# Kernel tuning notes

Hardware: AMD Instinct MI355X
Metric: run time of the kernel (lower is better)

Reference implementation:

```python
import jax, jax.numpy as jnp
import numpy as np

BLK = 128            # weight_block_size for w8a16 blockwise dequant
H = 1024             # hidden_size
I = 512              # moe_intermediate_size
E = 64               # n_routed_experts
T = 512              # tokens (seq_len)
K = 6                # num_experts_per_tok
G = 8                # n_group
TG = 3               # topk_group
NSH = 2              # n_shared_experts
I2 = I * NSH         # shared expert intermediate size
ROUTED_SCALE = 2.5
NORM_TOPK = True


def dq(w_int8, scale, blk=BLK):
    """Blockwise w8a16 dequant: w [..., M, N] int8, scale [..., M/blk, N/blk] f32."""
    *lead, M, N = w_int8.shape
    w = w_int8.astype(scale.dtype).reshape(*lead, M // blk, blk, N // blk, blk)
    return (w * scale[..., :, None, :, None]).reshape(*lead, M, N)


def setup_inputs() -> dict:
    key = jax.random.key(0)
    ks = jax.random.split(key, 16)
    ri = lambda k, shp: jax.random.randint(k, shp, -8, 8, dtype=jnp.int8)
    rs = lambda k, shp: jax.random.uniform(k, shp, minval=0.01, maxval=0.03, dtype=jnp.float32)
    return {
        "x": jax.random.normal(ks[0], (T, H), jnp.float32),
        "gate_w": jax.random.normal(ks[1], (E, H), jnp.float32) * 0.02,  # router gate [E,H]
        "wg": ri(ks[2], (E, I, H)),  "sg": rs(ks[3], (E, I // BLK, H // BLK)),
        "wu": ri(ks[4], (E, I, H)),  "su": rs(ks[5], (E, I // BLK, H // BLK)),
        "wd": ri(ks[6], (E, I, H)),  "sd": rs(ks[7], (E, I // BLK, H // BLK)),  # down, transposed layout [I,H]
        "sh_wg": ri(ks[8], (I2, H)),  "sh_sg": rs(ks[9], (I2 // BLK, H // BLK)),
        "sh_wu": ri(ks[10], (I2, H)), "sh_su": rs(ks[11], (I2 // BLK, H // BLK)),
        "sh_wd": ri(ks[12], (I2, H)), "sh_sd": rs(ks[13], (I2 // BLK, H // BLK)),
    }


def _moe(x, gate_w, wg, sg, wu, su, wd, sd, sh_wg, sh_sg, sh_wu, sh_su, sh_wd, sh_sd):
    Tn = x.shape[0]
    # --- router: sigmoid scoring + group-limited top-k ---
    scores = jax.nn.sigmoid(x @ gate_w.T)                       # [T, E]
    gsz = E // G
    group_scores = scores.reshape(Tn, G, gsz).max(axis=-1)      # [T, G]
    _, gidx = jax.lax.top_k(group_scores, TG)                   # [T, TG]
    gmask = jax.nn.one_hot(gidx, G, dtype=scores.dtype).sum(1)  # [T, G]
    emask = jnp.repeat(gmask, gsz, axis=-1)                     # [T, E]
    masked = jnp.where(emask > 0, scores, -jnp.inf)
    w, idx = jax.lax.top_k(masked, K)                           # [T, K]
    if NORM_TOPK:
        w = w / (w.sum(-1, keepdims=True) + 1e-20)
    w = w * ROUTED_SCALE
    # per-token combine weights over experts
    comb = (jax.nn.one_hot(idx, E, dtype=x.dtype) * w[:, :, None]).sum(1)  # [T, E]

    # --- routed experts: dequantized silu-gated MLPs, masked dense combine ---
    Wg, Wu, Wd = dq(wg, sg), dq(wu, su), dq(wd, sd)             # [E, I, H]
    g = jnp.einsum('th,eih->eti', x, Wg)                        # [E, T, I]
    u = jnp.einsum('th,eih->eti', x, Wu)
    hmid = jax.nn.silu(g) * u
    y = jnp.einsum('eti,eih->eth', hmid, Wd)                    # [E, T, H]
    routed = jnp.einsum('eth,te->th', y, comb)                  # [T, H]

    # --- shared experts MLP ---
    Sg, Su, Sd = dq(sh_wg, sh_sg), dq(sh_wu, sh_su), dq(sh_wd, sh_sd)
    shared = (jax.nn.silu(x @ Sg.T) * (x @ Su.T)) @ Sd          # [T, H]
    return routed + shared


def reference(x, gate_w, wg, sg, wu, su, wd, sd, sh_wg, sh_sg, sh_wu, sh_su, sh_wd, sh_sd):
    return _moe(x, gate_w, wg, sg, wu, su, wd, sd,
                sh_wg, sh_sg, sh_wu, sh_su, sh_wd, sh_sd)
```

## Files before the change

### kernel.cpp

```cpp
#include <hip/hip_runtime.h>
#include <math.h>
#include <stdint.h>

#define T_   512
#define H_   1024
#define I_   512
#define E_   64
#define K_   6
#define G_   8
#define TG_  3
#define EB_  80

typedef _Float16 h8 __attribute__((ext_vector_type(8)));
typedef _Float16 h4v __attribute__((ext_vector_type(4)));
typedef float    f4 __attribute__((ext_vector_type(4)));

__global__ __launch_bounds__(64) void router_k(
    const float* __restrict__ x, const float* __restrict__ gw,
    int* __restrict__ cnt, int* __restrict__ tlist, float* __restrict__ wlist)
{
  const int t   = blockIdx.x;
  const int tid = threadIdx.x;
  __shared__ float sx[H_];
  __shared__ float sc[E_];

  for (int h4 = tid; h4 < H_/4; h4 += 64)
    ((float4*)sx)[h4] = ((const float4*)(x + (size_t)t*H_))[h4];
  __syncthreads();

  const float* wr = gw + (size_t)tid * H_;
  float acc = 0.f;
  for (int h = 0; h < H_; h += 4) {
    float4 xv = *(const float4*)(sx + h);
    float4 wv = *(const float4*)(wr + h);
    acc = fmaf(xv.x, wv.x, acc); acc = fmaf(xv.y, wv.y, acc);
    acc = fmaf(xv.z, wv.z, acc); acc = fmaf(xv.w, wv.w, acc);
  }
  sc[tid] = 1.f / (1.f + expf(-acc));
  __syncthreads();

  if (tid == 0) {
    float gs[G_];
    #pragma unroll
    for (int g = 0; g < G_; g++) {
      float m = sc[g*8];
      #pragma unroll
      for (int j = 1; j < 8; j++) m = fmaxf(m, sc[g*8+j]);
      gs[g] = m;
    }
    unsigned gp = 0;
    for (int r = 0; r < TG_; r++) {
      int best = 0; float bv = -1e30f;
      for (int g = 0; g < G_; g++)
        if (!((gp >> g) & 1) && gs[g] > bv) { bv = gs[g]; best = g; }
      gp |= 1u << best;
    }
    int   eidx[K_]; float ew[K_];
    unsigned long long em = 0ull;
    float wsum = 0.f;
    for (int r = 0; r < K_; r++) {
      int best = 0; float bv = -1e30f;
      for (int e = 0; e < E_; e++) {
        if (!((gp >> (e >> 3)) & 1)) continue;
        if ((em >> e) & 1ull) continue;
        if (sc[e] > bv) { bv = sc[e]; best = e; }
      }
      em |= 1ull << best; eidx[r] = best; ew[r] = bv; wsum += bv;
    }
    const float inv = 2.5f / (wsum + 1e-20f);
    for (int r = 0; r < K_; r++) {
      int e = eidx[r];
      int pos = atomicAdd(&cnt[e], 1);
      tlist[e*T_ + pos] = (t << 13) | (t*K_ + r);
      wlist[e*T_ + pos] = ew[r] * inv;
    }
  }
}

__global__ void pseudo_init_k(int* cnt, int* tlist, float* wlist) {
  int s = blockIdx.x*256 + threadIdx.x;
  if (s == 0) { cnt[64] = T_; cnt[65] = T_; }
  if (s < 1024) {
    int e = 64 + (s >> 9);
    int t = s & 511;
    tlist[e*T_ + t] = (t << 13) | (3072 + s);
    wlist[e*T_ + t] = 1.0f;
  }
}

__global__ __launch_bounds__(256) void xh_prep_k(
    const float* __restrict__ x, _Float16* __restrict__ xh)
{
  int i = blockIdx.x*256 + threadIdx.x;
  float4 v = ((const float4*)x)[i];
  h4v o = { (_Float16)v.x, (_Float16)v.y, (_Float16)v.z, (_Float16)v.w };
  *(h4v*)(xh + (size_t)i*4) = o;
}

__device__ __forceinline__ void eb_decode(int eb, const int* cnt,
                                          int& e, int& lo, int& hi) {
  if (eb < E_) { e = eb; lo = 0; hi = cnt[e]; }
  else { int q = (eb - E_) & 7; e = E_ + ((eb - E_) >> 3); lo = q*64; hi = lo + 64; }
}

__device__ __forceinline__ h8 cvt8(int4 a, int4 b, float s) {
  union { _Float16 f[8]; h8 v; } t;
  t.f[0]=(_Float16)((float)a.x*s); t.f[1]=(_Float16)((float)a.y*s);
  t.f[2]=(_Float16)((float)a.z*s); t.f[3]=(_Float16)((float)a.w*s);
  t.f[4]=(_Float16)((float)b.x*s); t.f[5]=(_Float16)((float)b.y*s);
  t.f[6]=(_Float16)((float)b.z*s); t.f[7]=(_Float16)((float)b.w*s);
  return t.v;
}

#define NKT_G 32

#define GU_STEP(KT, WN)                                                       \
  do {                                                                        \
    asm volatile("s_waitcnt vmcnt(" #WN ") lgkmcnt(0)" ::: "memory");         \
    __builtin_amdgcn_sched_barrier(0);                                        \
    __builtin_amdgcn_s_barrier();                                             \
    __builtin_amdgcn_sched_barrier(0);                                        \
    if ((KT) + 1 < NKT_G)                                                     \
      *(h8*)(wdst + (((KT)+1)&1)*5120) =                                      \
          cvt8(Wr[((KT)+1)%3][0], Wr[((KT)+1)%3][1], sv[((KT)+1)>>2]);        \
    if ((KT) + 3 < NKT_G) {                                                   \
      Wr[((KT)+3)%3][0] = *(const int4*)(wsrc + ((KT)+3)*32);                 \
      Wr[((KT)+3)%3][1] = *(const int4*)(wsrc + ((KT)+3)*32 + 4);             \
    }                                                                         \
    {                                                                         \
      const _Float16* tb = lds0 + ((KT)&1)*5120;                              \
      h8 bg0 = *(const h8*)(tb + ro0);                                        \
      h8 bg1 = *(const h8*)(tb + ro1);                                        \
      h8 bu0 = *(const h8*)(tb + 2560 + ro0);                                 \
      h8 bu1 = *(const h8*)(tb + 2560 + ro1);                                 \
      accg0 = __builtin_amdgcn_mfma_f32_16x16x32_f16(Ar[(KT)%4], bg0, accg0, 0,0,0); \
      accg1 = __builtin_amdgcn_mfma_f32_16x16x32_f16(Ar[(KT)%4], bg1, accg1, 0,0,0); \
      accu0 = __builtin_amdgcn_mfma_f32_16x16x32_f16(Ar[(KT)%4], bu0, accu0, 0,0,0); \
      accu1 = __builtin_amdgcn_mfma_f32_16x16x32_f16(Ar[(KT)%4], bu1, accu1, 0,0,0); \
    }                                                                         \
    if ((KT) + 3 < NKT_G)                                                     \
      Ar[((KT)+3)%4] = *(const h8*)(ax + ((KT)+3)*32);                        \
  } while (0)

__global__ __launch_bounds__(512, 6) void gateup_k(
    const _Float16* __restrict__ xh,
    const int* __restrict__ wg, const float* __restrict__ sg,
    const int* __restrict__ wu, const float* __restrict__ su,
    const int* __restrict__ shwg, const float* __restrict__ shsg,
    const int* __restrict__ shwu, const float* __restrict__ shsu,
    const int* __restrict__ cnt, const int* __restrict__ tlist,
    const float* __restrict__ wlist,
    _Float16* __restrict__ hmid)
{
  const int ic = blockIdx.x;
  const int eb = blockIdx.y;
  int e, lo, hi;
  eb_decode(eb, cnt, e, lo, hi);
  if (hi <= lo) return;

  const int tid  = threadIdx.x;
  const int lane = tid & 63;
  const int wv   = tid >> 6;
  const int mr   = lane & 15;
  const int quad = lane >> 4;
  const int wm   = wv & 3;
  const int wn   = wv >> 2;

  const int *wgb, *wub; const float *sgp, *sup; int sib;
  if (e < E_) {
    wgb = wg + (size_t)e*I_*H_;  wub = wu + (size_t)e*I_*H_;
    sgp = sg + e*32;  sup = su + e*32;  sib = ic >> 1;
  } else {
    int hf = e - E_;
    wgb = shwg + (size_t)hf*512*H_;  wub = shwu + (size_t)hf*512*H_;
    sgp = shsg;  sup = shsu;  sib = hf*4 + (ic >> 1);
  }

  const int smat = tid >> 8;
  const int sr   = (tid >> 2) & 63;
  const int sseg = tid & 3;
  const int* wsrc = (smat ? wub : wgb) + (size_t)(ic*64 + sr)*H_ + sseg*8;
  const float* ssc = (smat ? sup : sgp) + sib*8;
  float sv[8];
  #pragma unroll
  for (int b = 0; b < 8; b++) sv[b] = ssc[b];

  __shared__ _Float16 wlds[2*2*64*40];
  __shared__ int stok[64]; __shared__ int srw[64]; __shared__ float swt[64];
  _Float16* lds0 = wlds;
  _Float16* wdst = wlds + smat*2560 + sr*40 + sseg*8;
  const int ro0 = (wn*32 + mr)*40 + quad*8;
  const int ro1 = ro0 + 16*40;

  int4 Wr[3][2];
  h8   Ar[4];

  for (int base = lo; base < hi; base += 64) {
    __syncthreads();
    if (tid < 64) {
      int slot = base + tid;
      if (slot < hi) {
        int ent = tlist[e*T_ + slot];
        stok[tid] = ent >> 13; srw[tid] = ent & 8191; swt[tid] = wlist[e*T_ + slot];
      } else { stok[tid] = -1; srw[tid] = 0; swt[tid] = 0.f; }
    }
    __syncthreads();

    int tk = stok[wm*16 + mr]; if (tk < 0) tk = 0;
    const _Float16* ax = xh + (size_t)tk*H_ + quad*8;

    f4 accg0 = (f4){0.f,0.f,0.f,0.f}, accg1 = accg0, accu0 = accg0, accu1 = accg0;

    Wr[0][0] = *(const int4*)(wsrc);      Wr[0][1] = *(const int4*)(wsrc + 4);
    Ar[0]    = *(const h8*)(ax);
    Wr[1][0] = *(const int4*)(wsrc + 32); Wr[1][1] = *(const int4*)(wsrc + 36);
    Ar[1]    = *(const h8*)(ax + 32);
    Wr[2][0] = *(const int4*)(wsrc + 64); Wr[2][1] = *(const int4*)(wsrc + 68);
    Ar[2]    = *(const h8*)(ax + 64);
    asm volatile("s_waitcnt vmcnt(7)" ::: "memory");
    __builtin_amdgcn_sched_barrier(0);
    *(h8*)(wdst) = cvt8(Wr[0][0], Wr[0][1], sv[0]);

    GU_STEP(0,4);  GU_STEP(1,4);  GU_STEP(2,4);  GU_STEP(3,4);
    GU_STEP(4,4);  GU_STEP(5,4);  GU_STEP(6,4);  GU_STEP(7,4);
    GU_STEP(8,4);  GU_STEP(9,4);  GU_STEP(10,4); GU_STEP(11,4);
    GU_STEP(12,4); GU_STEP(13,4); GU_STEP(14,4); GU_STEP(15,4);
    GU_STEP(16,4); GU_STEP(17,4); GU_STEP(18,4); GU_STEP(19,4);
    GU_STEP(20,4); GU_STEP(21,4); GU_STEP(22,4); GU_STEP(23,4);
    GU_STEP(24,4); GU_STEP(25,4); GU_STEP(26,4); GU_STEP(27,4);
    GU_STEP(28,4); GU_STEP(29,4); GU_STEP(30,1); GU_STEP(31,0);

    const int icol = ic*64 + wn*32 + mr;
    #pragma unroll
    for (int r = 0; r < 4; r++) {
      int sl = wm*16 + quad*4 + r;
      if (stok[sl] >= 0) {
        float wt = swt[sl];
        float g0 = accg0[r];
        float m0 = g0 / (1.f + expf(-g0)) * accu0[r] * wt;
        float g1 = accg1[r];
        float m1 = g1 / (1.f + expf(-g1)) * accu1[r] * wt;
        _Float16* hp = hmid + (size_t)srw[sl]*I_ + icol;
        hp[0]  = (_Float16)m0;
        hp[16] = (_Float16)m1;
      }
    }
  }
}
#undef GU_STEP

#define NKT_D 16

#define DN_LDW(S, KT)                                                         \
  do {                                                                        \
    Wr[S][0] = *(const int2*)(dsrc + (size_t)((KT)*32 + 0)*H_);               \
    Wr[S][1] = *(const int2*)(dsrc + (size_t)((KT)*32 + 1)*H_);               \
    Wr[S][2] = *(const int2*)(dsrc + (size_t)((KT)*32 + 2)*H_);               \
    Wr[S][3] = *(const int2*)(dsrc + (size_t)((KT)*32 + 3)*H_);               \
  } while (0)

#define DN_WRITE(S, BUF, SC)                                                  \
  do {                                                                        \
    union { _Float16 f[4]; h4v v; } v0, v1;                                   \
    v0.f[0]=(_Float16)((float)Wr[S][0].x*(SC)); v0.f[1]=(_Float16)((float)Wr[S][1].x*(SC)); \
    v0.f[2]=(_Float16)((float)Wr[S][2].x*(SC)); v0.f[3]=(_Float16)((float)Wr[S][3].x*(SC)); \
    v1.f[0]=(_Float16)((float)Wr[S][0].y*(SC)); v1.f[1]=(_Float16)((float)Wr[S][1].y*(SC)); \
    v1.f[2]=(_Float16)((float)Wr[S][2].y*(SC)); v1.f[3]=(_Float16)((float)Wr[S][3].y*(SC)); \
    *(h4v*)(ddst0 + (BUF)*2560)      = v0.v;                                  \
    *(h4v*)(ddst0 + (BUF)*2560 + 40) = v1.v;                                  \
  } while (0)

#define DN_STEP(KT, WN)                                                       \
  do {                                                                        \
    asm volatile("s_waitcnt vmcnt(" #WN ") lgkmcnt(0)" ::: "memory");         \
    __builtin_amdgcn_sched_barrier(0);                                        \
    __builtin_amdgcn_s_barrier();                                             \
    __builtin_amdgcn_sched_barrier(0);                                        \
    if ((KT) + 1 < NKT_D) DN_WRITE(((KT)+1)%3, ((KT)+1)&1, scd[((KT)+1)>>2]); \
    if ((KT) + 3 < NKT_D) DN_LDW(((KT)+3)%3, (KT)+3);                         \
    {                                                                         \
      const _Float16* tb = lds0 + ((KT)&1)*2560;                              \
      h8 b0 = *(const h8*)(tb + ro0);                                         \
      h8 b1 = *(const h8*)(tb + ro1);                                         \
      h8 b2 = *(const h8*)(tb + ro2);                                         \
      h8 b3 = *(const h8*)(tb + ro3);                                         \
      tot0 = __builtin_amdgcn_mfma_f32_16x16x32_f16(Ar[(KT)%4], b0, tot0, 0,0,0); \
      tot1 = __builtin_amdgcn_mfma_f32_16x16x32_f16(Ar[(KT)%4], b1, tot1, 0,0,0); \
      tot2 = __builtin_amdgcn_mfma_f32_16x16x32_f16(Ar[(KT)%4], b2, tot2, 0,0,0); \
      tot3 = __builtin_amdgcn_mfma_f32_16x16x32_f16(Ar[(KT)%4], b3, tot3, 0,0,0); \
    }                                                                         \
    if ((KT) + 3 < NKT_D)                                                     \
      Ar[((KT)+3)%4] = *(const h8*)(ap + ((KT)+3)*32);                        \
  } while (0)

__global__ __launch_bounds__(256, 6) void down_k(
    const int* __restrict__ wd, const float* __restrict__ sd,
    const int* __restrict__ shwd, const float* __restrict__ shsd,
    const int* __restrict__ cnt, const int* __restrict__ tlist,
    const _Float16* __restrict__ hmid, float* __restrict__ scr)
{
  const int hc = blockIdx.x;
  const int eb = blockIdx.y;
  int e, lo, hi;
  eb_decode(eb, cnt, e, lo, hi);
  if (hi <= lo) return;

  const int tid  = threadIdx.x;
  const int lane = tid & 63;
  const int wv   = tid >> 6;
  const int mr   = lane & 15;
  const int quad = lane >> 4;

  const int* wb; const float* sdp; int sib0;
  if (e < E_) { wb = wd + (size_t)e*I_*H_;        sdp = sd + e*32;  sib0 = 0; }
  else { int hf = e - E_; wb = shwd + (size_t)hf*512*H_; sdp = shsd; sib0 = hf*4; }
  float scd[4];
  #pragma unroll
  for (int ib = 0; ib < 4; ib++) scd[ib] = sdp[(sib0+ib)*8 + (hc >> 1)];

  const int ig = tid >> 5;
  const int hp = tid & 31;
  const int* dsrc = wb + (size_t)(ig*4)*H_ + hc*64 + hp*2;

  __shared__ _Float16 wlds[2*64*40];
  __shared__ int stok[64]; __shared__ int srw[64];
  _Float16* lds0  = wlds;
  _Float16* ddst0 = wlds + (hp*2)*40 + ig*4;
  const int ro0 = (     mr)*40 + quad*8;
  const int ro1 = (16 + mr)*40 + quad*8;
  const int ro2 = (32 + mr)*40 + quad*8;
  const int ro3 = (48 + mr)*40 + quad*8;

  int2 Wr[3][4];
  h8   Ar[4];

  for (int base = lo; base < hi; base += 64) {
    __syncthreads();
    if (tid < 64) {
      int slot = base + tid;
      if (slot < hi) {
        int ent = tlist[e*T_ + slot];
        stok[tid] = ent >> 13; srw[tid] = ent & 8191;
      } else { stok[tid] = -1; srw[tid] = 0; }
    }
    __syncthreads();

    const _Float16* ap = hmid + (size_t)srw[wv*16 + mr]*I_ + quad*8;

    f4 tot0 = (f4){0.f,0.f,0.f,0.f}, tot1 = tot0, tot2 = tot0, tot3 = tot0;

    DN_LDW(0, 0); Ar[0] = *(const h8*)(ap);
    DN_LDW(1, 1); Ar[1] = *(const h8*)(ap + 32);
    DN_LDW(2, 2); Ar[2] = *(const h8*)(ap + 64);
    asm volatile("s_waitcnt vmcnt(10)" ::: "memory");
    __builtin_amdgcn_sched_barrier(0);
    DN_WRITE(0, 0, scd[0]);

    DN_STEP(0,6);  DN_STEP(1,6);  DN_STEP(2,6);  DN_STEP(3,6);
    DN_STEP(4,6);  DN_STEP(5,6);  DN_STEP(6,6);  DN_STEP(7,6);
    DN_STEP(8,6);  DN_STEP(9,6);  DN_STEP(10,6); DN_STEP(11,6);
    DN_STEP(12,6); DN_STEP(13,6); DN_STEP(14,1); DN_STEP(15,0);

    #pragma unroll
    for (int r = 0; r < 4; r++) {
      int sl = wv*16 + quad*4 + r;
      if (stok[sl] >= 0) {
        int t  = stok[sl];
        int sr = srw[sl];
        int rank = (sr < 3072) ? (sr - t*6) : (6 + ((sr - 3072) >> 9));
        float* dst = scr + (size_t)(t*8 + rank)*H_ + hc*64 + mr;
        dst[0]  = tot0[r];
        dst[16] = tot1[r];
        dst[32] = tot2[r];
        dst[48] = tot3[r];
      }
    }
  }
}
#undef DN_STEP
#undef DN_WRITE
#undef DN_LDW

__global__ __launch_bounds__(256) void combine_k(
    const float* __restrict__ scr, float* __restrict__ out)
{
  int i = blockIdx.x*256 + threadIdx.x;
  int t = i >> 8;
  int c = i & 255;
  const float4* base = (const float4*)(scr + (size_t)t*8*H_) + c;
  float4 s = base[0];
  #pragma unroll
  for (int r = 1; r < 8; r++) {
    float4 v = base[(size_t)r*(H_/4)];
    s.x += v.x; s.y += v.y; s.z += v.z; s.w += v.w;
  }
  ((float4*)out)[i] = s;
}

extern "C" void kernel_launch(void* const* d_in, const int* in_sizes, int n_in,
                              void* d_out, int out_size, void* d_ws, size_t ws_size,
                              hipStream_t stream) {
  (void)in_sizes; (void)n_in; (void)ws_size; (void)out_size;
  const float* x    = (const float*)d_in[0];
  const float* gw   = (const float*)d_in[1];
  const int*   wg   = (const int*  )d_in[2];
  const float* sg   = (const float*)d_in[3];
  const int*   wu   = (const int*  )d_in[4];
  const float* su   = (const float*)d_in[5];
  const int*   wd   = (const int*  )d_in[6];
  const float* sd   = (const float*)d_in[7];
  const int*   shwg = (const int*  )d_in[8];
  const float* shsg = (const float*)d_in[9];
  const int*   shwu = (const int*  )d_in[10];
  const float* shsu = (const float*)d_in[11];
  const int*   shwd = (const int*  )d_in[12];
  const float* shsd = (const float*)d_in[13];
  float* out = (float*)d_out;

  char* ws = (char*)d_ws;
  int*      cnt   = (int*     ) ws;
  int*      tlist = (int*     )(ws + 1024);
  float*    wlist = (float*   )(ws + 1024 + 66*T_*4);
  _Float16* hmid  = (_Float16*)(ws + 1024 + 2*66*T_*4);
  _Float16* xh    = (_Float16*)(ws + 1024 + 2*66*T_*4 + 4096*I_*2);
  float*    scr   = (float*   )(ws + 1024 + 2*66*T_*4 + 4096*I_*2 + T_*H_*2);

  hipMemsetAsync(cnt, 0, 1024, stream);
  xh_prep_k<<<T_*H_/1024, 256, 0, stream>>>(x, xh);
  router_k<<<T_, 64, 0, stream>>>(x, gw, cnt, tlist, wlist);
  pseudo_init_k<<<4, 256, 0, stream>>>(cnt, tlist, wlist);
  gateup_k<<<dim3(8, EB_), 512, 0, stream>>>(xh, wg, sg, wu, su,
                                             shwg, shsg, shwu, shsu,
                                             cnt, tlist, wlist, hmid);
  down_k<<<dim3(16, EB_), 256, 0, stream>>>(wd, sd, shwd, shsd,
                                            cnt, tlist, hmid, scr);
  combine_k<<<T_*H_/1024, 256, 0, stream>>>(scr, out);
}
```

Before: 557.3 us.

## Halve gate/up and down column tiles and fold prep kernels into router

Gate/up blocks now cover 32 intermediate columns instead of 64, and down blocks cover 32 hidden columns instead of 64. Each launch therefore has twice as many blocks with fewer accumulators and registers each, and the occupancy hint rises to 8. The fp16 conversion of x and the shared-expert pseudo-routing setup move into the router kernel, which removes two launches. Routing weights are now stored per (token, rank) row instead of per expert slot. In exchange, each block rereads the activation tiles for fewer output columns, which raises redundant A-operand traffic and the number of barriers per FLOP.

```diff
diff --git a/kernel.cpp b/kernel.cpp
--- a/kernel.cpp
+++ b/kernel.cpp
@@ -13,11 +13,13 @@
 
 typedef _Float16 h8 __attribute__((ext_vector_type(8)));
 typedef _Float16 h4v __attribute__((ext_vector_type(4)));
+typedef _Float16 h2v __attribute__((ext_vector_type(2)));
 typedef float    f4 __attribute__((ext_vector_type(4)));
 
 __global__ __launch_bounds__(64) void router_k(
     const float* __restrict__ x, const float* __restrict__ gw,
-    int* __restrict__ cnt, int* __restrict__ tlist, float* __restrict__ wlist)
+    int* __restrict__ cnt, int* __restrict__ tlist,
+    float* __restrict__ wrow, _Float16* __restrict__ xh)
 {
   const int t   = blockIdx.x;
   const int tid = threadIdx.x;
@@ -27,6 +29,20 @@
   for (int h4 = tid; h4 < H_/4; h4 += 64)
     ((float4*)sx)[h4] = ((const float4*)(x + (size_t)t*H_))[h4];
   __syncthreads();
+
+  for (int h4 = tid; h4 < H_/4; h4 += 64) {
+    float4 v = ((const float4*)sx)[h4];
+    h4v o = { (_Float16)v.x, (_Float16)v.y, (_Float16)v.z, (_Float16)v.w };
+    *(h4v*)(xh + (size_t)t*H_ + h4*4) = o;
+  }
+  if (t < 16) {
+    int s  = t*64 + tid;
+    int e  = 64 + (s >> 9);
+    int tt = s & 511;
+    tlist[e*T_ + tt] = (tt << 13) | (3072 + s);
+    wrow[3072 + s] = 1.0f;
+    if (s == 0) { cnt[64] = T_; cnt[65] = T_; }
+  }
 
   const float* wr = gw + (size_t)tid * H_;
   float acc = 0.f;
@@ -72,29 +88,9 @@
       int e = eidx[r];
       int pos = atomicAdd(&cnt[e], 1);
       tlist[e*T_ + pos] = (t << 13) | (t*K_ + r);
-      wlist[e*T_ + pos] = ew[r] * inv;
-    }
-  }
-}
-
-__global__ void pseudo_init_k(int* cnt, int* tlist, float* wlist) {
-  int s = blockIdx.x*256 + threadIdx.x;
-  if (s == 0) { cnt[64] = T_; cnt[65] = T_; }
-  if (s < 1024) {
-    int e = 64 + (s >> 9);
-    int t = s & 511;
-    tlist[e*T_ + t] = (t << 13) | (3072 + s);
-    wlist[e*T_ + t] = 1.0f;
-  }
-}
-
-__global__ __launch_bounds__(256) void xh_prep_k(
-    const float* __restrict__ x, _Float16* __restrict__ xh)
-{
-  int i = blockIdx.x*256 + threadIdx.x;
-  float4 v = ((const float4*)x)[i];
-  h4v o = { (_Float16)v.x, (_Float16)v.y, (_Float16)v.z, (_Float16)v.w };
-  *(h4v*)(xh + (size_t)i*4) = o;
+      wrow[t*K_ + r] = ew[r] * inv;
+    }
+  }
 }
 
 __device__ __forceinline__ void eb_decode(int eb, const int* cnt,
@@ -103,13 +99,10 @@
   else { int q = (eb - E_) & 7; e = E_ + ((eb - E_) >> 3); lo = q*64; hi = lo + 64; }
 }
 
-__device__ __forceinline__ h8 cvt8(int4 a, int4 b, float s) {
-  union { _Float16 f[8]; h8 v; } t;
-  t.f[0]=(_Float16)((float)a.x*s); t.f[1]=(_Float16)((float)a.y*s);
-  t.f[2]=(_Float16)((float)a.z*s); t.f[3]=(_Float16)((float)a.w*s);
-  t.f[4]=(_Float16)((float)b.x*s); t.f[5]=(_Float16)((float)b.y*s);
-  t.f[6]=(_Float16)((float)b.z*s); t.f[7]=(_Float16)((float)b.w*s);
-  return t.v;
+__device__ __forceinline__ h4v cvt4i(int4 w, float s) {
+  h4v t = { (_Float16)((float)w.x*s), (_Float16)((float)w.y*s),
+            (_Float16)((float)w.z*s), (_Float16)((float)w.w*s) };
+  return t;
 }
 
 #define NKT_G 32
@@ -121,38 +114,32 @@
     __builtin_amdgcn_s_barrier();                                             \
     __builtin_amdgcn_sched_barrier(0);                                        \
     if ((KT) + 1 < NKT_G)                                                     \
-      *(h8*)(wdst + (((KT)+1)&1)*5120) =                                      \
-          cvt8(Wr[((KT)+1)%3][0], Wr[((KT)+1)%3][1], sv[((KT)+1)>>2]);        \
-    if ((KT) + 3 < NKT_G) {                                                   \
-      Wr[((KT)+3)%3][0] = *(const int4*)(wsrc + ((KT)+3)*32);                 \
-      Wr[((KT)+3)%3][1] = *(const int4*)(wsrc + ((KT)+3)*32 + 4);             \
-    }                                                                         \
+      *(h4v*)(wdst + (((KT)+1)&1)*2560) =                                     \
+          cvt4i(Wr[((KT)+1)%3], sv[((KT)+1)>>2]);                             \
+    if ((KT) + 3 < NKT_G)                                                     \
+      Wr[((KT)+3)%3] = *(const int4*)(wsrc + ((KT)+3)*32);                    \
     {                                                                         \
-      const _Float16* tb = lds0 + ((KT)&1)*5120;                              \
-      h8 bg0 = *(const h8*)(tb + ro0);                                        \
-      h8 bg1 = *(const h8*)(tb + ro1);                                        \
-      h8 bu0 = *(const h8*)(tb + 2560 + ro0);                                 \
-      h8 bu1 = *(const h8*)(tb + 2560 + ro1);                                 \
-      accg0 = __builtin_amdgcn_mfma_f32_16x16x32_f16(Ar[(KT)%4], bg0, accg0, 0,0,0); \
-      accg1 = __builtin_amdgcn_mfma_f32_16x16x32_f16(Ar[(KT)%4], bg1, accg1, 0,0,0); \
-      accu0 = __builtin_amdgcn_mfma_f32_16x16x32_f16(Ar[(KT)%4], bu0, accu0, 0,0,0); \
-      accu1 = __builtin_amdgcn_mfma_f32_16x16x32_f16(Ar[(KT)%4], bu1, accu1, 0,0,0); \
+      const _Float16* tb = lds0 + ((KT)&1)*2560;                              \
+      h8 bg = *(const h8*)(tb + ro0);                                         \
+      h8 bu = *(const h8*)(tb + 1280 + ro0);                                  \
+      accg = __builtin_amdgcn_mfma_f32_16x16x32_f16(Ar[(KT)%4], bg, accg, 0,0,0); \
+      accu = __builtin_amdgcn_mfma_f32_16x16x32_f16(Ar[(KT)%4], bu, accu, 0,0,0); \
     }                                                                         \
     if ((KT) + 3 < NKT_G)                                                     \
       Ar[((KT)+3)%4] = *(const h8*)(ax + ((KT)+3)*32);                        \
   } while (0)
 
-__global__ __launch_bounds__(512, 6) void gateup_k(
+__global__ __launch_bounds__(512, 8) void gateup_k(
     const _Float16* __restrict__ xh,
     const int* __restrict__ wg, const float* __restrict__ sg,
     const int* __restrict__ wu, const float* __restrict__ su,
     const int* __restrict__ shwg, const float* __restrict__ shsg,
     const int* __restrict__ shwu, const float* __restrict__ shsu,
     const int* __restrict__ cnt, const int* __restrict__ tlist,
-    const float* __restrict__ wlist,
+    const float* __restrict__ wrow,
     _Float16* __restrict__ hmid)
 {
-  const int ic = blockIdx.x;
+  const int bi = blockIdx.x;
   const int eb = blockIdx.y;
   int e, lo, hi;
   eb_decode(eb, cnt, e, lo, hi);
@@ -169,30 +156,29 @@
   const int *wgb, *wub; const float *sgp, *sup; int sib;
   if (e < E_) {
     wgb = wg + (size_t)e*I_*H_;  wub = wu + (size_t)e*I_*H_;
-    sgp = sg + e*32;  sup = su + e*32;  sib = ic >> 1;
+    sgp = sg + e*32;  sup = su + e*32;  sib = bi >> 2;
   } else {
     int hf = e - E_;
     wgb = shwg + (size_t)hf*512*H_;  wub = shwu + (size_t)hf*512*H_;
-    sgp = shsg;  sup = shsu;  sib = hf*4 + (ic >> 1);
+    sgp = shsg;  sup = shsu;  sib = hf*4 + (bi >> 2);
   }
 
   const int smat = tid >> 8;
-  const int sr   = (tid >> 2) & 63;
-  const int sseg = tid & 3;
-  const int* wsrc = (smat ? wub : wgb) + (size_t)(ic*64 + sr)*H_ + sseg*8;
+  const int sr   = (tid >> 3) & 31;
+  const int seg  = tid & 7;
+  const int* wsrc = (smat ? wub : wgb) + (size_t)(bi*32 + sr)*H_ + seg*4;
   const float* ssc = (smat ? sup : sgp) + sib*8;
   float sv[8];
   #pragma unroll
   for (int b = 0; b < 8; b++) sv[b] = ssc[b];
 
-  __shared__ _Float16 wlds[2*2*64*40];
+  __shared__ _Float16 wlds[2*2*32*40];
   __shared__ int stok[64]; __shared__ int srw[64]; __shared__ float swt[64];
   _Float16* lds0 = wlds;
-  _Float16* wdst = wlds + smat*2560 + sr*40 + sseg*8;
-  const int ro0 = (wn*32 + mr)*40 + quad*8;
-  const int ro1 = ro0 + 16*40;
-
-  int4 Wr[3][2];
+  _Float16* wdst = wlds + smat*1280 + sr*40 + seg*4;
+  const int ro0 = (wn*16 + mr)*40 + quad*8;
+
+  int4 Wr[3];
   h8   Ar[4];
 
   for (int base = lo; base < hi; base += 64) {
@@ -201,7 +187,8 @@
       int slot = base + tid;
       if (slot < hi) {
         int ent = tlist[e*T_ + slot];
-        stok[tid] = ent >> 13; srw[tid] = ent & 8191; swt[tid] = wlist[e*T_ + slot];
+        stok[tid] = ent >> 13; srw[tid] = ent & 8191;
+        swt[tid]  = wrow[ent & 8191];
       } else { stok[tid] = -1; srw[tid] = 0; swt[tid] = 0.f; }
     }
     __syncthreads();
@@ -209,40 +196,33 @@
     int tk = stok[wm*16 + mr]; if (tk < 0) tk = 0;
     const _Float16* ax = xh + (size_t)tk*H_ + quad*8;
 
-    f4 accg0 = (f4){0.f,0.f,0.f,0.f}, accg1 = accg0, accu0 = accg0, accu1 = accg0;
-
-    Wr[0][0] = *(const int4*)(wsrc);      Wr[0][1] = *(const int4*)(wsrc + 4);
-    Ar[0]    = *(const h8*)(ax);
-    Wr[1][0] = *(const int4*)(wsrc + 32); Wr[1][1] = *(const int4*)(wsrc + 36);
-    Ar[1]    = *(const h8*)(ax + 32);
-    Wr[2][0] = *(const int4*)(wsrc + 64); Wr[2][1] = *(const int4*)(wsrc + 68);
-    Ar[2]    = *(const h8*)(ax + 64);
-    asm volatile("s_waitcnt vmcnt(7)" ::: "memory");
+    f4 accg = (f4){0.f,0.f,0.f,0.f}, accu = accg;
+
+    Wr[0] = *(const int4*)(wsrc);        Ar[0] = *(const h8*)(ax);
+    Wr[1] = *(const int4*)(wsrc + 32);   Ar[1] = *(const h8*)(ax + 32);
+    Wr[2] = *(const int4*)(wsrc + 64);   Ar[2] = *(const h8*)(ax + 64);
+    asm volatile("s_waitcnt vmcnt(5)" ::: "memory");
     __builtin_amdgcn_sched_barrier(0);
-    *(h8*)(wdst) = cvt8(Wr[0][0], Wr[0][1], sv[0]);
-
-    GU_STEP(0,4);  GU_STEP(1,4);  GU_STEP(2,4);  GU_STEP(3,4);
-    GU_STEP(4,4);  GU_STEP(5,4);  GU_STEP(6,4);  GU_STEP(7,4);
-    GU_STEP(8,4);  GU_STEP(9,4);  GU_STEP(10,4); GU_STEP(11,4);
-    GU_STEP(12,4); GU_STEP(13,4); GU_STEP(14,4); GU_STEP(15,4);
-    GU_STEP(16,4); GU_STEP(17,4); GU_STEP(18,4); GU_STEP(19,4);
-    GU_STEP(20,4); GU_STEP(21,4); GU_STEP(22,4); GU_STEP(23,4);
-    GU_STEP(24,4); GU_STEP(25,4); GU_STEP(26,4); GU_STEP(27,4);
-    GU_STEP(28,4); GU_STEP(29,4); GU_STEP(30,1); GU_STEP(31,0);
-
-    const int icol = ic*64 + wn*32 + mr;
+    *(h4v*)(wdst) = cvt4i(Wr[0], sv[0]);
+
+    GU_STEP(0,3);  GU_STEP(1,3);  GU_STEP(2,3);  GU_STEP(3,3);
+    GU_STEP(4,3);  GU_STEP(5,3);  GU_STEP(6,3);  GU_STEP(7,3);
+    GU_STEP(8,3);  GU_STEP(9,3);  GU_STEP(10,3); GU_STEP(11,3);
+    GU_STEP(12,3); GU_STEP(13,3); GU_STEP(14,3); GU_STEP(15,3);
+    GU_STEP(16,3); GU_STEP(17,3); GU_STEP(18,3); GU_STEP(19,3);
+    GU_STEP(20,3); GU_STEP(21,3); GU_STEP(22,3); GU_STEP(23,3);
+    GU_STEP(24,3); GU_STEP(25,3); GU_STEP(26,3); GU_STEP(27,3);
+    GU_STEP(28,3); GU_STEP(29,3); GU_STEP(30,1); GU_STEP(31,0);
+
+    const int icol = bi*32 + wn*16 + mr;
     #pragma unroll
     for (int r = 0; r < 4; r++) {
       int sl = wm*16 + quad*4 + r;
       if (stok[sl] >= 0) {
         float wt = swt[sl];
-        float g0 = accg0[r];
-        float m0 = g0 / (1.f + expf(-g0)) * accu0[r] * wt;
-        float g1 = accg1[r];
-        float m1 = g1 / (1.f + expf(-g1)) * accu1[r] * wt;
-        _Float16* hp = hmid + (size_t)srw[sl]*I_ + icol;
-        hp[0]  = (_Float16)m0;
-        hp[16] = (_Float16)m1;
+        float g0 = accg[r];
+        float m0 = g0 / (1.f + expf(-g0)) * accu[r] * wt;
+        hmid[(size_t)srw[sl]*I_ + icol] = (_Float16)m0;
       }
     }
   }
@@ -255,19 +235,16 @@
   do {                                                                        \
     Wr[S][0] = *(const int2*)(dsrc + (size_t)((KT)*32 + 0)*H_);               \
     Wr[S][1] = *(const int2*)(dsrc + (size_t)((KT)*32 + 1)*H_);               \
-    Wr[S][2] = *(const int2*)(dsrc + (size_t)((KT)*32 + 2)*H_);               \
-    Wr[S][3] = *(const int2*)(dsrc + (size_t)((KT)*32 + 3)*H_);               \
   } while (0)
 
 #define DN_WRITE(S, BUF, SC)                                                  \
   do {                                                                        \
-    union { _Float16 f[4]; h4v v; } v0, v1;                                   \
-    v0.f[0]=(_Float16)((float)Wr[S][0].x*(SC)); v0.f[1]=(_Float16)((float)Wr[S][1].x*(SC)); \
-    v0.f[2]=(_Float16)((float)Wr[S][2].x*(SC)); v0.f[3]=(_Float16)((float)Wr[S][3].x*(SC)); \
-    v1.f[0]=(_Float16)((float)Wr[S][0].y*(SC)); v1.f[1]=(_Float16)((float)Wr[S][1].y*(SC)); \
-    v1.f[2]=(_Float16)((float)Wr[S][2].y*(SC)); v1.f[3]=(_Float16)((float)Wr[S][3].y*(SC)); \
-    *(h4v*)(ddst0 + (BUF)*2560)      = v0.v;                                  \
-    *(h4v*)(ddst0 + (BUF)*2560 + 40) = v1.v;                                  \
+    h2v v0 = { (_Float16)((float)Wr[S][0].x*(SC)),                            \
+               (_Float16)((float)Wr[S][1].x*(SC)) };                          \
+    h2v v1 = { (_Float16)((float)Wr[S][0].y*(SC)),                            \
+               (_Float16)((float)Wr[S][1].y*(SC)) };                          \
+    *(h2v*)(ddst0 + (BUF)*1280)      = v0;                                    \
+    *(h2v*)(ddst0 + (BUF)*1280 + 40) = v1;                                    \
   } while (0)
 
 #define DN_STEP(KT, WN)                                                       \
@@ -279,21 +256,17 @@
     if ((KT) + 1 < NKT_D) DN_WRITE(((KT)+1)%3, ((KT)+1)&1, scd[((KT)+1)>>2]); \
     if ((KT) + 3 < NKT_D) DN_LDW(((KT)+3)%3, (KT)+3);                         \
     {                                                                         \
-      const _Float16* tb = lds0 + ((KT)&1)*2560;                              \
+      const _Float16* tb = lds0 + ((KT)&1)*1280;                              \
       h8 b0 = *(const h8*)(tb + ro0);                                         \
       h8 b1 = *(const h8*)(tb + ro1);                                         \
-      h8 b2 = *(const h8*)(tb + ro2);                                         \
-      h8 b3 = *(const h8*)(tb + ro3);                                         \
       tot0 = __builtin_amdgcn_mfma_f32_16x16x32_f16(Ar[(KT)%4], b0, tot0, 0,0,0); \
       tot1 = __builtin_amdgcn_mfma_f32_16x16x32_f16(Ar[(KT)%4], b1, tot1, 0,0,0); \
-      tot2 = __builtin_amdgcn_mfma_f32_16x16x32_f16(Ar[(KT)%4], b2, tot2, 0,0,0); \
-      tot3 = __builtin_amdgcn_mfma_f32_16x16x32_f16(Ar[(KT)%4], b3, tot3, 0,0,0); \
     }                                                                         \
     if ((KT) + 3 < NKT_D)                                                     \
       Ar[((KT)+3)%4] = *(const h8*)(ap + ((KT)+3)*32);                        \
   } while (0)
 
-__global__ __launch_bounds__(256, 6) void down_k(
+__global__ __launch_bounds__(256, 8) void down_k(
     const int* __restrict__ wd, const float* __restrict__ sd,
     const int* __restrict__ shwd, const float* __restrict__ shsd,
     const int* __restrict__ cnt, const int* __restrict__ tlist,
@@ -316,22 +289,20 @@
   else { int hf = e - E_; wb = shwd + (size_t)hf*512*H_; sdp = shsd; sib0 = hf*4; }
   float scd[4];
   #pragma unroll
-  for (int ib = 0; ib < 4; ib++) scd[ib] = sdp[(sib0+ib)*8 + (hc >> 1)];
-
-  const int ig = tid >> 5;
-  const int hp = tid & 31;
-  const int* dsrc = wb + (size_t)(ig*4)*H_ + hc*64 + hp*2;
-
-  __shared__ _Float16 wlds[2*64*40];
+  for (int ib = 0; ib < 4; ib++) scd[ib] = sdp[(sib0+ib)*8 + (hc >> 2)];
+
+  const int ig = tid >> 4;
+  const int hp = tid & 15;
+  const int* dsrc = wb + (size_t)(ig*2)*H_ + hc*32 + hp*2;
+
+  __shared__ _Float16 wlds[2*32*40];
   __shared__ int stok[64]; __shared__ int srw[64];
   _Float16* lds0  = wlds;
-  _Float16* ddst0 = wlds + (hp*2)*40 + ig*4;
+  _Float16* ddst0 = wlds + (hp*2)*40 + ig*2;
   const int ro0 = (     mr)*40 + quad*8;
   const int ro1 = (16 + mr)*40 + quad*8;
-  const int ro2 = (32 + mr)*40 + quad*8;
-  const int ro3 = (48 + mr)*40 + quad*8;
-
-  int2 Wr[3][4];
+
+  int2 Wr[3][2];
   h8   Ar[4];
 
   for (int base = lo; base < hi; base += 64) {
@@ -347,19 +318,19 @@
 
     const _Float16* ap = hmid + (size_t)srw[wv*16 + mr]*I_ + quad*8;
 
-    f4 tot0 = (f4){0.f,0.f,0.f,0.f}, tot1 = tot0, tot2 = tot0, tot3 = tot0;
+    f4 tot0 = (f4){0.f,0.f,0.f,0.f}, tot1 = tot0;
 
     DN_LDW(0, 0); Ar[0] = *(const h8*)(ap);
     DN_LDW(1, 1); Ar[1] = *(const h8*)(ap + 32);
     DN_LDW(2, 2); Ar[2] = *(const h8*)(ap + 64);
-    asm volatile("s_waitcnt vmcnt(10)" ::: "memory");
+    asm volatile("s_waitcnt vmcnt(7)" ::: "memory");
     __builtin_amdgcn_sched_barrier(0);
     DN_WRITE(0, 0, scd[0]);
 
-    DN_STEP(0,6);  DN_STEP(1,6);  DN_STEP(2,6);  DN_STEP(3,6);
-    DN_STEP(4,6);  DN_STEP(5,6);  DN_STEP(6,6);  DN_STEP(7,6);
-    DN_STEP(8,6);  DN_STEP(9,6);  DN_STEP(10,6); DN_STEP(11,6);
-    DN_STEP(12,6); DN_STEP(13,6); DN_STEP(14,1); DN_STEP(15,0);
+    DN_STEP(0,4);  DN_STEP(1,4);  DN_STEP(2,4);  DN_STEP(3,4);
+    DN_STEP(4,4);  DN_STEP(5,4);  DN_STEP(6,4);  DN_STEP(7,4);
+    DN_STEP(8,4);  DN_STEP(9,4);  DN_STEP(10,4); DN_STEP(11,4);
+    DN_STEP(12,4); DN_STEP(13,4); DN_STEP(14,1); DN_STEP(15,0);
 
     #pragma unroll
     for (int r = 0; r < 4; r++) {
@@ -368,11 +339,9 @@
         int t  = stok[sl];
         int sr = srw[sl];
         int rank = (sr < 3072) ? (sr - t*6) : (6 + ((sr - 3072) >> 9));
-        float* dst = scr + (size_t)(t*8 + rank)*H_ + hc*64 + mr;
+        float* dst = scr + (size_t)(t*8 + rank)*H_ + hc*32 + mr;
         dst[0]  = tot0[r];
         dst[16] = tot1[r];
-        dst[32] = tot2[r];
-        dst[48] = tot3[r];
       }
     }
   }
@@ -420,19 +389,17 @@
   char* ws = (char*)d_ws;
   int*      cnt   = (int*     ) ws;
   int*      tlist = (int*     )(ws + 1024);
-  float*    wlist = (float*   )(ws + 1024 + 66*T_*4);
-  _Float16* hmid  = (_Float16*)(ws + 1024 + 2*66*T_*4);
-  _Float16* xh    = (_Float16*)(ws + 1024 + 2*66*T_*4 + 4096*I_*2);
-  float*    scr   = (float*   )(ws + 1024 + 2*66*T_*4 + 4096*I_*2 + T_*H_*2);
+  float*    wrow  = (float*   )(ws + 136192);
+  _Float16* hmid  = (_Float16*)(ws + 152576);
+  _Float16* xh    = (_Float16*)(ws + 4346880);
+  float*    scr   = (float*   )(ws + 5395456);
 
   hipMemsetAsync(cnt, 0, 1024, stream);
-  xh_prep_k<<<T_*H_/1024, 256, 0, stream>>>(x, xh);
-  router_k<<<T_, 64, 0, stream>>>(x, gw, cnt, tlist, wlist);
-  pseudo_init_k<<<4, 256, 0, stream>>>(cnt, tlist, wlist);
-  gateup_k<<<dim3(8, EB_), 512, 0, stream>>>(xh, wg, sg, wu, su,
-                                             shwg, shsg, shwu, shsu,
-                                             cnt, tlist, wlist, hmid);
-  down_k<<<dim3(16, EB_), 256, 0, stream>>>(wd, sd, shwd, shsd,
+  router_k<<<T_, 64, 0, stream>>>(x, gw, cnt, tlist, wrow, xh);
+  gateup_k<<<dim3(16, EB_), 512, 0, stream>>>(xh, wg, sg, wu, su,
+                                              shwg, shsg, shwu, shsu,
+                                              cnt, tlist, wrow, hmid);
+  down_k<<<dim3(32, EB_), 256, 0, stream>>>(wd, sd, shwd, shsd,
                                             cnt, tlist, hmid, scr);
-  combine_k<<<T_*H_/1024, 256, 0, stream>>>(scr, out);
-}
+  combine_k<<<512, 256, 0, stream>>>(scr, out);
+}
```

New measurement: 539.7 us. 1.03x faster.
